# Kernel optimization log

Hardware: AMD Instinct MI355X
Metric: run time of the kernel (lower is better)

## Reference

```python
import jax, jax.numpy as jnp
import numpy as np

B, T, C, H = 8, 2048, 512, 512


def setup_inputs() -> dict:
    key = jax.random.key(0)
    ks = jax.random.split(key, 9)
    s = 1.0 / np.sqrt(C)
    return {
        "q": jax.random.normal(ks[0], (B, T, C), jnp.float32),
        "k": jax.random.normal(ks[1], (B, T, C), jnp.float32),
        "v": jax.random.normal(ks[2], (B, T, C), jnp.float32),
        "Wq": jax.random.normal(ks[3], (C, H), jnp.float32) * s,
        "bq": jax.random.normal(ks[4], (H,), jnp.float32) * 0.01,
        "Wk": jax.random.normal(ks[5], (C, H), jnp.float32) * s,
        "bk": jax.random.normal(ks[6], (H,), jnp.float32) * 0.01,
        "Wv": jax.random.normal(ks[7], (C, H), jnp.float32) * s,
        "bv": jax.random.normal(ks[8], (H,), jnp.float32) * 0.01,
    }


def reference(q, k, v, Wq, bq, Wk, bk, Wv, bv):
    # Linear projections (Real_Linear == nn.Linear): [B,T,C] @ [C,H] + [H]
    query = jnp.einsum('btc,ch->bth', q, Wq) + bq
    key_p = jnp.einsum('btc,ch->bth', k, Wk) + bk
    value = jnp.einsum('btc,ch->bth', v, Wv) + bv
    # energy = Q @ K^T / sqrt(H)  -> [B, T, T]
    energy = jnp.einsum('bth,byh->bty', query, key_p) / jnp.sqrt(jnp.asarray(H, query.dtype))
    attn = jax.nn.softmax(energy, axis=-1)
    # weighted value: [B, T, T] @ [B, T, H] -> [B, T, H]
    return jnp.einsum('bty,byh->bth', attn, value)
```

## Files before the change

### kernel.cpp

```cpp
#include <hip/hip_runtime.h>
#include <hip/hip_bf16.h>

typedef unsigned short u16;
typedef unsigned int u32;
typedef short s16x8 __attribute__((ext_vector_type(8)));
typedef float f32x4 __attribute__((ext_vector_type(4)));

#define NB 8
#define NT 2048
#define NC 512
#define NH 512

__device__ __forceinline__ u16 f2bf(float f) {
  unsigned u = __float_as_uint(f);
  u += 0x7FFFu + ((u >> 16) & 1u);
  return (u16)(u >> 16);
}

__device__ __forceinline__ void gld16(const u16* src, u16* lds_dst) {
  __builtin_amdgcn_global_load_lds(
      (const __attribute__((address_space(1))) u32*)src,
      (__attribute__((address_space(3))) u32*)lds_dst, 16, 0, 0);
}

__global__ __launch_bounds__(256) void wt_kernel(const float* __restrict__ Wq,
                                                 const float* __restrict__ Wk,
                                                 const float* __restrict__ Wv,
                                                 u16* __restrict__ WqT,
                                                 u16* __restrict__ WkT,
                                                 u16* __restrict__ WvT) {
  __shared__ float tile[32][33];
  const float* W = (blockIdx.z == 0) ? Wq : (blockIdx.z == 1) ? Wk : Wv;
  u16* WT = (blockIdx.z == 0) ? WqT : (blockIdx.z == 1) ? WkT : WvT;
  const int x = threadIdx.x & 31;
  const int y = threadIdx.x >> 5;
  const int k0 = blockIdx.x * 32, h0 = blockIdx.y * 32;
#pragma unroll
  for (int p = 0; p < 4; ++p)
    tile[y + 8 * p][x] = W[(size_t)(k0 + y + 8 * p) * NH + h0 + x];
  __syncthreads();
#pragma unroll
  for (int p = 0; p < 4; ++p)
    WT[(size_t)(h0 + y + 8 * p) * NC + k0 + x] = f2bf(tile[x][y + 8 * p]);
}

__global__ __launch_bounds__(256) void proj_kernel(const float* __restrict__ Xq,
                                                   const float* __restrict__ Xk,
                                                   const float* __restrict__ Xv,
                                                   const u16* __restrict__ WqT,
                                                   const u16* __restrict__ WkT,
                                                   const u16* __restrict__ WvT,
                                                   const float* __restrict__ bq,
                                                   const float* __restrict__ bk,
                                                   const float* __restrict__ bv,
                                                   u16* __restrict__ Yq,
                                                   u16* __restrict__ Yk,
                                                   u16* __restrict__ Yv) {
  __shared__ __align__(16) u16 Asub[2][128 * 40];
  __shared__ __align__(16) u16 Bsub[2][128 * 40];
  const int zz = blockIdx.z;
  const float* X = (zz == 0) ? Xq : (zz == 1) ? Xk : Xv;
  const u16* WT = (zz == 0) ? WqT : (zz == 1) ? WkT : WvT;
  const float* bias = (zz == 0) ? bq : (zz == 1) ? bk : bv;
  u16* Y = (zz == 0) ? Yq : (zz == 1) ? Yk : Yv;

  const int t = threadIdx.x;
  const int lane = t & 63;
  const int w = t >> 6;
  const int l16 = lane & 15;
  const int ko8 = (lane >> 4) * 8;
  const int m0 = blockIdx.y * 128;
  const int n0 = blockIdx.x * 128;
  const int wr = (w >> 1) * 64, wc = (w & 1) * 64;
  f32x4 acc[4][4] = {};

  float4 areg[4];
  int4 breg[2];
#define PLOAD(kt)                                                              \
  {                                                                            \
    const int k0_ = (kt) * 32;                                                 \
    _Pragma("unroll")                                                          \
    for (int p = 0; p < 4; ++p) {                                              \
      int c = t + 256 * p;                                                     \
      areg[p] = *(const float4*)&X[(size_t)(m0 + (c >> 3)) * NC + k0_ + (c & 7) * 4]; \
    }                                                                          \
    _Pragma("unroll")                                                          \
    for (int p = 0; p < 2; ++p) {                                              \
      int c = t + 256 * p;                                                     \
      breg[p] = *(const int4*)&WT[(size_t)(n0 + (c >> 2)) * NC + k0_ + (c & 3) * 8];  \
    }                                                                          \
  }
#define PWRITE(buf)                                                            \
  {                                                                            \
    _Pragma("unroll")                                                          \
    for (int p = 0; p < 4; ++p) {                                              \
      int c = t + 256 * p;                                                     \
      ushort4 bb;                                                              \
      bb.x = f2bf(areg[p].x); bb.y = f2bf(areg[p].y);                          \
      bb.z = f2bf(areg[p].z); bb.w = f2bf(areg[p].w);                          \
      *(ushort4*)&Asub[buf][(c >> 3) * 40 + (c & 7) * 4] = bb;                 \
    }                                                                          \
    _Pragma("unroll")                                                          \
    for (int p = 0; p < 2; ++p) {                                              \
      int c = t + 256 * p;                                                     \
      *(int4*)&Bsub[buf][(c >> 2) * 40 + (c & 3) * 8] = breg[p];               \
    }                                                                          \
  }

  PLOAD(0)
  PWRITE(0)
  __syncthreads();

  int pb = 0;
  for (int kt = 0; kt < 16; ++kt) {
    if (kt < 15) PLOAD(kt + 1)
    s16x8 af[4], bf[4];
#pragma unroll
    for (int i = 0; i < 4; ++i)
      af[i] = *(const s16x8*)&Asub[pb][(wr + i * 16 + l16) * 40 + ko8];
#pragma unroll
    for (int j = 0; j < 4; ++j)
      bf[j] = *(const s16x8*)&Bsub[pb][(wc + j * 16 + l16) * 40 + ko8];
#pragma unroll
    for (int i = 0; i < 4; ++i)
#pragma unroll
      for (int j = 0; j < 4; ++j)
        acc[i][j] = __builtin_amdgcn_mfma_f32_16x16x32_bf16(af[i], bf[j], acc[i][j], 0, 0, 0);
    if (kt < 15) PWRITE(pb ^ 1)
    __syncthreads();
    pb ^= 1;
  }
#undef PLOAD
#undef PWRITE
  const int rg = (lane >> 4) * 4;
#pragma unroll
  for (int i = 0; i < 4; ++i)
#pragma unroll
    for (int j = 0; j < 4; ++j) {
      const int col = n0 + wc + j * 16 + l16;
      const float bcol = bias[col];
#pragma unroll
      for (int jj = 0; jj < 4; ++jj) {
        const int row = m0 + wr + i * 16 + rg + jj;
        Y[(size_t)row * NH + col] = f2bf(acc[i][j][jj] + bcol);
      }
    }
}

__global__ __launch_bounds__(256) void vt_kernel(const u16* __restrict__ Vp,
                                                 u16* __restrict__ VpT) {
  __shared__ u16 tile[32][33];
  const int x = threadIdx.x & 31;
  const int y = threadIdx.x >> 5;
  const int t0 = blockIdx.x * 32, h0 = blockIdx.y * 32, b = blockIdx.z;
  const u16* src = Vp + (size_t)b * NT * NH;
  u16* dst = VpT + (size_t)b * NH * NT;
#pragma unroll
  for (int p = 0; p < 4; ++p)
    tile[y + 8 * p][x] = src[(size_t)(t0 + y + 8 * p) * NH + h0 + x];
  __syncthreads();
#pragma unroll
  for (int p = 0; p < 4; ++p)
    dst[(size_t)(h0 + y + 8 * p) * NT + t0 + x] = tile[x][y + 8 * p];
}

__global__ __launch_bounds__(512, 2) void flash_partial(const u16* __restrict__ Qp,
                                                        const u16* __restrict__ Kp,
                                                        const u16* __restrict__ VpT,
                                                        float* __restrict__ O0,
                                                        float* __restrict__ O1,
                                                        float* __restrict__ mlws) {
  __shared__ __align__(16) u16 Klds[2][32 * 512];
  __shared__ __align__(16) u16 Vlds[2][32 * 512];

  const int t = threadIdx.x;
  const int lane = t & 63;
  const int w = t >> 6;
  const int l16 = lane & 15;
  const int g = lane >> 4;
  const int g8 = g * 8;
  const int b = blockIdx.x;
  const int q0 = blockIdx.y * 128;
  const int z = blockIdx.z;
  const int qg = q0 + w * 16 + l16;
  const int kperm = (l16 >> 2) * 8 + (l16 & 3);
  const float kscale = 0.044194173824159216f;

  s16x8 qf[16];
  {
    const u16* qrow = Qp + (size_t)(b * NT + qg) * NH;
#pragma unroll
    for (int ks = 0; ks < 16; ++ks)
      qf[ks] = *(const s16x8*)&qrow[ks * 32 + g8];
  }

  f32x4 oacc[32] = {};
  float m_run = -1e30f, l_run = 0.f;

  const u16* kbat = Kp + (size_t)(b * NT + z * 1024) * NH;
  const u16* vbat = VpT + (size_t)b * NH * NT + z * 1024;

#define STAGE(buf, it)                                                         \
  {                                                                            \
    _Pragma("unroll")                                                          \
    for (int r = 0; r < 4; ++r) {                                              \
      const int i = w * 4 + r;                                      \
      gld16(kbat + (size_t)((it) * 32 + kperm + ((i & 1) << 2)) * NH           \
                 + ((i >> 1) << 5) + g8,                                       \
            &Klds[buf][i * 512]);                                              \
      gld16(vbat + (size_t)(i * 16 + l16) * NT + (it) * 32 + g8,               \
            &Vlds[buf][i * 512]);                                              \
    }                                                                          \
  }

  STAGE(0, 0)
  __syncthreads();

  int pb = 0;
  for (int it = 0; it < 32; ++it) {
    if (it < 31) STAGE(pb ^ 1, it + 1)
    f32x4 s0a = {}, s0b = {}, s1a = {}, s1b = {};
    __builtin_amdgcn_s_setprio(1);
#pragma unroll
    for (int ks = 0; ks < 8; ++ks) {
      s16x8 kf0 = *(const s16x8*)&Klds[pb][(ks * 2 + 0) * 512 + lane * 8];
      s16x8 kf1 = *(const s16x8*)&Klds[pb][(ks * 2 + 1) * 512 + lane * 8];
      s16x8 kf2 = *(const s16x8*)&Klds[pb][((ks + 8) * 2 + 0) * 512 + lane * 8];
      s16x8 kf3 = *(const s16x8*)&Klds[pb][((ks + 8) * 2 + 1) * 512 + lane * 8];
      s0a = __builtin_amdgcn_mfma_f32_16x16x32_bf16(kf0, qf[ks], s0a, 0, 0, 0);
      s1a = __builtin_amdgcn_mfma_f32_16x16x32_bf16(kf1, qf[ks], s1a, 0, 0, 0);
      s0b = __builtin_amdgcn_mfma_f32_16x16x32_bf16(kf2, qf[ks + 8], s0b, 0, 0, 0);
      s1b = __builtin_amdgcn_mfma_f32_16x16x32_bf16(kf3, qf[ks + 8], s1b, 0, 0, 0);
    }
    __builtin_amdgcn_s_setprio(0);
    const f32x4 s0 = s0a + s0b;
    const f32x4 s1 = s1a + s1b;
    float pv[8];
#pragma unroll
    for (int j = 0; j < 4; ++j) { pv[j] = s0[j] * kscale; pv[4 + j] = s1[j] * kscale; }
    float mx = pv[0];
#pragma unroll
    for (int j = 1; j < 8; ++j) mx = fmaxf(mx, pv[j]);
    mx = fmaxf(mx, __shfl_xor(mx, 16, 64));
    mx = fmaxf(mx, __shfl_xor(mx, 32, 64));
    if (__any(mx > m_run + 8.f)) {
      const float m_new = fmaxf(m_run, mx);
      const float scale = __expf(m_run - m_new);
#pragma unroll
      for (int ht = 0; ht < 32; ++ht) {
        oacc[ht][0] *= scale; oacc[ht][1] *= scale;
        oacc[ht][2] *= scale; oacc[ht][3] *= scale;
      }
      l_run *= scale;
      m_run = m_new;
    }
    float ts = 0.f;
#pragma unroll
    for (int j = 0; j < 8; ++j) { pv[j] = __expf(pv[j] - m_run); ts += pv[j]; }
    l_run += ts;
    union { u32 u[4]; s16x8 v; } pf;
    pf.u[0] = ((u32)f2bf(pv[1]) << 16) | f2bf(pv[0]);
    pf.u[1] = ((u32)f2bf(pv[3]) << 16) | f2bf(pv[2]);
    pf.u[2] = ((u32)f2bf(pv[5]) << 16) | f2bf(pv[4]);
    pf.u[3] = ((u32)f2bf(pv[7]) << 16) | f2bf(pv[6]);
    __builtin_amdgcn_s_setprio(1);
#pragma unroll
    for (int ht = 0; ht < 32; ++ht) {
      s16x8 vf = *(const s16x8*)&Vlds[pb][ht * 512 + lane * 8];
      oacc[ht] = __builtin_amdgcn_mfma_f32_16x16x32_bf16(vf, pf.v, oacc[ht], 0, 0, 0);
    }
    __builtin_amdgcn_s_setprio(0);
    __syncthreads();
    pb ^= 1;
  }
  float* obase = (z ? O1 : O0) + (size_t)(b * NT + qg) * NH;
#pragma unroll
  for (int ht = 0; ht < 32; ++ht) {
    float4 st;
    st.x = oacc[ht][0]; st.y = oacc[ht][1];
    st.z = oacc[ht][2]; st.w = oacc[ht][3];
    *(float4*)&obase[ht * 16 + g * 4] = st;
  }
  float lt = l_run;
  lt += __shfl_xor(lt, 16, 64);
  lt += __shfl_xor(lt, 32, 64);
  if (g == 0) {
    const size_t row = (size_t)b * NT + qg;
    mlws[row * 4 + z * 2 + 0] = m_run;
    mlws[row * 4 + z * 2 + 1] = lt;
  }
#undef STAGE
}

__global__ __launch_bounds__(256) void merge_kernel(float* __restrict__ out,
                                                    const float* __restrict__ O1,
                                                    const float* __restrict__ mlws) {
  const size_t row = (size_t)blockIdx.x * 2 + (threadIdx.x >> 7);
  const int col4 = (threadIdx.x & 127) * 4;
  const float m0 = mlws[row * 4 + 0], l0 = mlws[row * 4 + 1];
  const float m1 = mlws[row * 4 + 2], l1 = mlws[row * 4 + 3];
  const float m = fmaxf(m0, m1);
  const float a0 = __expf(m0 - m), a1 = __expf(m1 - m);
  const float inv = 1.f / (a0 * l0 + a1 * l1);
  const float c0 = a0 * inv, c1 = a1 * inv;
  const size_t idx = row * NH + col4;
  float4 o0 = *(const float4*)&out[idx];
  float4 o1 = *(const float4*)&O1[idx];
  float4 r;
  r.x = c0 * o0.x + c1 * o1.x;
  r.y = c0 * o0.y + c1 * o1.y;
  r.z = c0 * o0.z + c1 * o1.z;
  r.w = c0 * o0.w + c1 * o1.w;
  *(float4*)&out[idx] = r;
}

__global__ __launch_bounds__(256, 1) void flash_kernel(const u16* __restrict__ Qp,
                                                       const u16* __restrict__ Kp,
                                                       const u16* __restrict__ VpT,
                                                       float* __restrict__ out) {
  __shared__ __align__(16) u16 Klds[2][32 * 512];
  __shared__ __align__(16) u16 Vlds[2][32 * 512];

  const int t = threadIdx.x;
  const int lane = t & 63;
  const int w = t >> 6;
  const int l16 = lane & 15;
  const int g = lane >> 4;
  const int g8 = g * 8;
  const int b = blockIdx.x;
  const int q0 = blockIdx.y * 64;
  const int qg = q0 + w * 16 + l16;
  const int kperm = (l16 >> 2) * 8 + (l16 & 3);
  const float kscale = 0.044194173824159216f;

  s16x8 qf[16];
  {
    const u16* qrow = Qp + (size_t)(b * NT + qg) * NH;
#pragma unroll
    for (int ks = 0; ks < 16; ++ks)
      qf[ks] = *(const s16x8*)&qrow[ks * 32 + g8];
  }
  f32x4 oacc[32] = {};
  float m_run = -1e30f, l_run = 0.f;
  const u16* kbat = Kp + (size_t)b * NT * NH;
  const u16* vbat = VpT + (size_t)b * NH * NT;

#pragma unroll
  for (int r = 0; r < 8; ++r) {
    const int i = w * 8 + r;
    gld16(kbat + (size_t)(kperm + ((i & 1) << 2)) * NH + ((i >> 1) << 5) + g8,
          &Klds[0][i * 512]);
    gld16(vbat + (size_t)(i * 16 + l16) * NT + g8, &Vlds[0][i * 512]);
  }
  __syncthreads();

  int pb = 0;
  for (int it = 0; it < 64; ++it) {
    if (it < 63) {
      const int kv1 = (it + 1) * 32;
      const int nb = pb ^ 1;
#pragma unroll
      for (int r = 0; r < 8; ++r) {
        const int i = w * 8 + r;
        gld16(kbat + (size_t)(kv1 + kperm + ((i & 1) << 2)) * NH + ((i >> 1) << 5) + g8,
              &Klds[nb][i * 512]);
        gld16(vbat + (size_t)(i * 16 + l16) * NT + kv1 + g8, &Vlds[nb][i * 512]);
      }
    }
    f32x4 s0 = {}, s1 = {};
#pragma unroll
    for (int ks = 0; ks < 16; ++ks) {
      s16x8 kf0 = *(const s16x8*)&Klds[pb][(ks * 2 + 0) * 512 + lane * 8];
      s16x8 kf1 = *(const s16x8*)&Klds[pb][(ks * 2 + 1) * 512 + lane * 8];
      s0 = __builtin_amdgcn_mfma_f32_16x16x32_bf16(kf0, qf[ks], s0, 0, 0, 0);
      s1 = __builtin_amdgcn_mfma_f32_16x16x32_bf16(kf1, qf[ks], s1, 0, 0, 0);
    }
    float pv[8];
#pragma unroll
    for (int j = 0; j < 4; ++j) { pv[j] = s0[j] * kscale; pv[4 + j] = s1[j] * kscale; }
    float mx = pv[0];
#pragma unroll
    for (int j = 1; j < 8; ++j) mx = fmaxf(mx, pv[j]);
    mx = fmaxf(mx, __shfl_xor(mx, 16, 64));
    mx = fmaxf(mx, __shfl_xor(mx, 32, 64));
    if (__any(mx > m_run + 8.f)) {
      const float m_new = fmaxf(m_run, mx);
      const float scale = __expf(m_run - m_new);
#pragma unroll
      for (int ht = 0; ht < 32; ++ht) {
        oacc[ht][0] *= scale; oacc[ht][1] *= scale;
        oacc[ht][2] *= scale; oacc[ht][3] *= scale;
      }
      l_run *= scale;
      m_run = m_new;
    }
    float ts = 0.f;
#pragma unroll
    for (int j = 0; j < 8; ++j) { pv[j] = __expf(pv[j] - m_run); ts += pv[j]; }
    l_run += ts;
    union { u32 u[4]; s16x8 v; } pf;
    pf.u[0] = ((u32)f2bf(pv[1]) << 16) | f2bf(pv[0]);
    pf.u[1] = ((u32)f2bf(pv[3]) << 16) | f2bf(pv[2]);
    pf.u[2] = ((u32)f2bf(pv[5]) << 16) | f2bf(pv[4]);
    pf.u[3] = ((u32)f2bf(pv[7]) << 16) | f2bf(pv[6]);
#pragma unroll
    for (int ht = 0; ht < 32; ++ht) {
      s16x8 vf = *(const s16x8*)&Vlds[pb][ht * 512 + lane * 8];
      oacc[ht] = __builtin_amdgcn_mfma_f32_16x16x32_bf16(vf, pf.v, oacc[ht], 0, 0, 0);
    }
    __syncthreads();
    pb ^= 1;
  }
  float lt = l_run;
  lt += __shfl_xor(lt, 16, 64);
  lt += __shfl_xor(lt, 32, 64);
  const float inv = 1.f / lt;
  float* obase = out + (size_t)(b * NT + qg) * NH;
#pragma unroll
  for (int ht = 0; ht < 32; ++ht) {
    float4 st;
    st.x = oacc[ht][0] * inv; st.y = oacc[ht][1] * inv;
    st.z = oacc[ht][2] * inv; st.w = oacc[ht][3] * inv;
    *(float4*)&obase[ht * 16 + g * 4] = st;
  }
}

extern "C" void kernel_launch(void* const* d_in, const int* in_sizes, int n_in,
                              void* d_out, int out_size, void* d_ws, size_t ws_size,
                              hipStream_t stream) {
  (void)in_sizes; (void)n_in; (void)out_size;
  const float* q  = (const float*)d_in[0];
  const float* k  = (const float*)d_in[1];
  const float* v  = (const float*)d_in[2];
  const float* Wq = (const float*)d_in[3];
  const float* bq = (const float*)d_in[4];
  const float* Wk = (const float*)d_in[5];
  const float* bk = (const float*)d_in[6];
  const float* Wv = (const float*)d_in[7];
  const float* bv = (const float*)d_in[8];
  float* out = (float*)d_out;

  u16* ws   = (u16*)d_ws;
  u16* WqT  = ws;
  u16* WkT  = WqT + (size_t)NC * NH;
  u16* WvT  = WkT + (size_t)NC * NH;
  u16* Qp   = WvT + (size_t)NC * NH;
  u16* Kp   = Qp + (size_t)NB * NT * NH;
  u16* Vp   = Kp + (size_t)NB * NT * NH;
  u16* VpT  = Vp + (size_t)NB * NT * NH;
  u16* endb = VpT + (size_t)NB * NT * NH;
  float* O1   = (float*)endb;
  float* mlws = O1 + (size_t)NB * NT * NH;
  const size_t need = (size_t)((char*)(mlws + (size_t)NB * NT * 4) - (char*)d_ws);

  wt_kernel<<<dim3(16, 16, 3), 256, 0, stream>>>(Wq, Wk, Wv, WqT, WkT, WvT);

  proj_kernel<<<dim3(4, 128, 3), 256, 0, stream>>>(q, k, v, WqT, WkT, WvT,
                                                   bq, bk, bv, Qp, Kp, Vp);

  vt_kernel<<<dim3(64, 16, NB), 256, 0, stream>>>(Vp, VpT);

  if (ws_size >= need) {
    flash_partial<<<dim3(NB, NT / 128, 2), 512, 0, stream>>>(Qp, Kp, VpT, out, O1, mlws);
    merge_kernel<<<dim3(NB * NT / 2), 256, 0, stream>>>(out, O1, mlws);
  } else {
    flash_kernel<<<dim3(NB, NT / 64), 256, 0, stream>>>(Qp, Kp, VpT, out);
  }
}
```

Before: 215.2 us.

## Switch flash attention to 32x32x16 MFMA with wave-pair split of head dimension

```diff
diff --git a/kernel.cpp b/kernel.cpp
--- a/kernel.cpp
+++ b/kernel.cpp
@@ -5,6 +5,7 @@
 typedef unsigned int u32;
 typedef short s16x8 __attribute__((ext_vector_type(8)));
 typedef float f32x4 __attribute__((ext_vector_type(4)));
+typedef float f32x16 __attribute__((ext_vector_type(16)));
 
 #define NB 8
 #define NT 2048
@@ -172,29 +173,32 @@
                                                         float* __restrict__ mlws) {
   __shared__ __align__(16) u16 Klds[2][32 * 512];
   __shared__ __align__(16) u16 Vlds[2][32 * 512];
+  __shared__ __align__(16) float Sx[8][1024];
 
   const int t = threadIdx.x;
   const int lane = t & 63;
   const int w = t >> 6;
-  const int l16 = lane & 15;
-  const int g = lane >> 4;
-  const int g8 = g * 8;
+  const int qgrp = w >> 1;
+  const int wh = w & 1;
+  const int l31 = lane & 31;
+  const int hi = lane >> 5;
   const int b = blockIdx.x;
   const int q0 = blockIdx.y * 128;
   const int z = blockIdx.z;
-  const int qg = q0 + w * 16 + l16;
-  const int kperm = (l16 >> 2) * 8 + (l16 & 3);
+  const int qg = q0 + qgrp * 32 + l31;
   const float kscale = 0.044194173824159216f;
+  const int kvr = ((l31 >> 4) & 1) * 16 + ((l31 >> 2) & 1) * 8 +
+                  ((l31 >> 3) & 1) * 4 + (l31 & 3);
 
   s16x8 qf[16];
   {
-    const u16* qrow = Qp + (size_t)(b * NT + qg) * NH;
-#pragma unroll
-    for (int ks = 0; ks < 16; ++ks)
-      qf[ks] = *(const s16x8*)&qrow[ks * 32 + g8];
-  }
-
-  f32x4 oacc[32] = {};
+    const u16* qrow = Qp + (size_t)(b * NT + qg) * NH + wh * 256 + hi * 8;
+#pragma unroll
+    for (int f = 0; f < 16; ++f)
+      qf[f] = *(const s16x8*)&qrow[f * 16];
+  }
+
+  f32x16 oacc[8] = {};
   float m_run = -1e30f, l_run = 0.f;
 
   const u16* kbat = Kp + (size_t)(b * NT + z * 1024) * NH;
@@ -203,13 +207,14 @@
 #define STAGE(buf, it)                                                         \
   {                                                                            \
     _Pragma("unroll")                                                          \
-    for (int r = 0; r < 4; ++r) {                                              \
-      const int i = w * 4 + r;                                      \
-      gld16(kbat + (size_t)((it) * 32 + kperm + ((i & 1) << 2)) * NH           \
-                 + ((i >> 1) << 5) + g8,                                       \
-            &Klds[buf][i * 512]);                                              \
-      gld16(vbat + (size_t)(i * 16 + l16) * NT + (it) * 32 + g8,               \
-            &Vlds[buf][i * 512]);                                              \
+    for (int r_ = 0; r_ < 4; ++r_) {                                           \
+      const int f = w * 4 + r_;                                     \
+      gld16(kbat + (size_t)((it) * 32 + kvr) * NH + f * 16 + hi * 8,           \
+            &Klds[buf][f * 512]);                                              \
+      const int whv = f >> 4, htv = (f >> 1) & 7, sv = f & 1;                  \
+      gld16(vbat + (size_t)(whv * 256 + htv * 32 + l31) * NT                   \
+                 + (it) * 32 + sv * 16 + hi * 8,                               \
+            &Vlds[buf][f * 512]);                                              \
     }                                                                          \
   }
 
@@ -219,72 +224,84 @@
   int pb = 0;
   for (int it = 0; it < 32; ++it) {
     if (it < 31) STAGE(pb ^ 1, it + 1)
-    f32x4 s0a = {}, s0b = {}, s1a = {}, s1b = {};
+    f32x16 sacc = {};
     __builtin_amdgcn_s_setprio(1);
 #pragma unroll
-    for (int ks = 0; ks < 8; ++ks) {
-      s16x8 kf0 = *(const s16x8*)&Klds[pb][(ks * 2 + 0) * 512 + lane * 8];
-      s16x8 kf1 = *(const s16x8*)&Klds[pb][(ks * 2 + 1) * 512 + lane * 8];
-      s16x8 kf2 = *(const s16x8*)&Klds[pb][((ks + 8) * 2 + 0) * 512 + lane * 8];
-      s16x8 kf3 = *(const s16x8*)&Klds[pb][((ks + 8) * 2 + 1) * 512 + lane * 8];
-      s0a = __builtin_amdgcn_mfma_f32_16x16x32_bf16(kf0, qf[ks], s0a, 0, 0, 0);
-      s1a = __builtin_amdgcn_mfma_f32_16x16x32_bf16(kf1, qf[ks], s1a, 0, 0, 0);
-      s0b = __builtin_amdgcn_mfma_f32_16x16x32_bf16(kf2, qf[ks + 8], s0b, 0, 0, 0);
-      s1b = __builtin_amdgcn_mfma_f32_16x16x32_bf16(kf3, qf[ks + 8], s1b, 0, 0, 0);
+    for (int f = 0; f < 16; ++f) {
+      s16x8 kf = *(const s16x8*)&Klds[pb][(wh * 16 + f) * 512 + lane * 8];
+      sacc = __builtin_amdgcn_mfma_f32_32x32x16_bf16(kf, qf[f], sacc, 0, 0, 0);
     }
     __builtin_amdgcn_s_setprio(0);
-    const f32x4 s0 = s0a + s0b;
-    const f32x4 s1 = s1a + s1b;
-    float pv[8];
-#pragma unroll
-    for (int j = 0; j < 4; ++j) { pv[j] = s0[j] * kscale; pv[4 + j] = s1[j] * kscale; }
+    {
+      float* myx = &Sx[w][0];
+#pragma unroll
+      for (int c = 0; c < 4; ++c) {
+        float4 tv;
+        tv.x = sacc[c * 4 + 0]; tv.y = sacc[c * 4 + 1];
+        tv.z = sacc[c * 4 + 2]; tv.w = sacc[c * 4 + 3];
+        *(float4*)&myx[c * 256 + lane * 4] = tv;
+      }
+    }
+    __syncthreads();
+    float pv[16];
+    {
+      const float* twx = &Sx[w ^ 1][0];
+#pragma unroll
+      for (int c = 0; c < 4; ++c) {
+        float4 tv = *(const float4*)&twx[c * 256 + lane * 4];
+        pv[c * 4 + 0] = (sacc[c * 4 + 0] + tv.x) * kscale;
+        pv[c * 4 + 1] = (sacc[c * 4 + 1] + tv.y) * kscale;
+        pv[c * 4 + 2] = (sacc[c * 4 + 2] + tv.z) * kscale;
+        pv[c * 4 + 3] = (sacc[c * 4 + 3] + tv.w) * kscale;
+      }
+    }
     float mx = pv[0];
 #pragma unroll
-    for (int j = 1; j < 8; ++j) mx = fmaxf(mx, pv[j]);
-    mx = fmaxf(mx, __shfl_xor(mx, 16, 64));
+    for (int j = 1; j < 16; ++j) mx = fmaxf(mx, pv[j]);
     mx = fmaxf(mx, __shfl_xor(mx, 32, 64));
     if (__any(mx > m_run + 8.f)) {
       const float m_new = fmaxf(m_run, mx);
       const float scale = __expf(m_run - m_new);
 #pragma unroll
-      for (int ht = 0; ht < 32; ++ht) {
-        oacc[ht][0] *= scale; oacc[ht][1] *= scale;
-        oacc[ht][2] *= scale; oacc[ht][3] *= scale;
-      }
+      for (int o = 0; o < 8; ++o) oacc[o] *= scale;
       l_run *= scale;
       m_run = m_new;
     }
     float ts = 0.f;
 #pragma unroll
-    for (int j = 0; j < 8; ++j) { pv[j] = __expf(pv[j] - m_run); ts += pv[j]; }
+    for (int j = 0; j < 16; ++j) { pv[j] = __expf(pv[j] - m_run); ts += pv[j]; }
     l_run += ts;
-    union { u32 u[4]; s16x8 v; } pf;
-    pf.u[0] = ((u32)f2bf(pv[1]) << 16) | f2bf(pv[0]);
-    pf.u[1] = ((u32)f2bf(pv[3]) << 16) | f2bf(pv[2]);
-    pf.u[2] = ((u32)f2bf(pv[5]) << 16) | f2bf(pv[4]);
-    pf.u[3] = ((u32)f2bf(pv[7]) << 16) | f2bf(pv[6]);
+    union { u32 u[4]; s16x8 v; } pf1, pf2;
+#pragma unroll
+    for (int c = 0; c < 4; ++c) {
+      pf1.u[c] = ((u32)f2bf(pv[c * 2 + 1]) << 16) | f2bf(pv[c * 2]);
+      pf2.u[c] = ((u32)f2bf(pv[8 + c * 2 + 1]) << 16) | f2bf(pv[8 + c * 2]);
+    }
     __builtin_amdgcn_s_setprio(1);
 #pragma unroll
-    for (int ht = 0; ht < 32; ++ht) {
-      s16x8 vf = *(const s16x8*)&Vlds[pb][ht * 512 + lane * 8];
-      oacc[ht] = __builtin_amdgcn_mfma_f32_16x16x32_bf16(vf, pf.v, oacc[ht], 0, 0, 0);
+    for (int ht = 0; ht < 8; ++ht) {
+      s16x8 vf1 = *(const s16x8*)&Vlds[pb][(wh * 16 + ht * 2 + 0) * 512 + lane * 8];
+      s16x8 vf2 = *(const s16x8*)&Vlds[pb][(wh * 16 + ht * 2 + 1) * 512 + lane * 8];
+      oacc[ht] = __builtin_amdgcn_mfma_f32_32x32x16_bf16(vf1, pf1.v, oacc[ht], 0, 0, 0);
+      oacc[ht] = __builtin_amdgcn_mfma_f32_32x32x16_bf16(vf2, pf2.v, oacc[ht], 0, 0, 0);
     }
     __builtin_amdgcn_s_setprio(0);
     __syncthreads();
     pb ^= 1;
   }
-  float* obase = (z ? O1 : O0) + (size_t)(b * NT + qg) * NH;
-#pragma unroll
-  for (int ht = 0; ht < 32; ++ht) {
-    float4 st;
-    st.x = oacc[ht][0]; st.y = oacc[ht][1];
-    st.z = oacc[ht][2]; st.w = oacc[ht][3];
-    *(float4*)&obase[ht * 16 + g * 4] = st;
-  }
-  float lt = l_run;
-  lt += __shfl_xor(lt, 16, 64);
-  lt += __shfl_xor(lt, 32, 64);
-  if (g == 0) {
+  float* obase = (z ? O1 : O0) + (size_t)(b * NT + qg) * NH + wh * 256;
+#pragma unroll
+  for (int ht = 0; ht < 8; ++ht) {
+#pragma unroll
+    for (int c = 0; c < 4; ++c) {
+      float4 st;
+      st.x = oacc[ht][c * 4 + 0]; st.y = oacc[ht][c * 4 + 1];
+      st.z = oacc[ht][c * 4 + 2]; st.w = oacc[ht][c * 4 + 3];
+      *(float4*)&obase[ht * 32 + c * 8 + hi * 4] = st;
+    }
+  }
+  float lt = l_run + __shfl_xor(l_run, 32, 64);
+  if (wh == 0 && hi == 0) {
     const size_t row = (size_t)b * NT + qg;
     mlws[row * 4 + z * 2 + 0] = m_run;
     mlws[row * 4 + z * 2 + 1] = lt;
```

Result: slower. 231.8 us (+7.7%).

## Shrink flash_partial to 64-query blocks with 16-key tiles and 16x16x16 PV MFMA

Applied to the files above, without the earlier changes.

```diff
diff --git a/kernel.cpp b/kernel.cpp
--- a/kernel.cpp
+++ b/kernel.cpp
@@ -4,12 +4,19 @@
 typedef unsigned short u16;
 typedef unsigned int u32;
 typedef short s16x8 __attribute__((ext_vector_type(8)));
+typedef short s16x4 __attribute__((ext_vector_type(4)));
 typedef float f32x4 __attribute__((ext_vector_type(4)));
 
 #define NB 8
 #define NT 2048
 #define NC 512
 #define NH 512
+
+#if __has_builtin(__builtin_amdgcn_mfma_f32_16x16x16_bf16)
+#define MFMA_PV(va, pb, c) __builtin_amdgcn_mfma_f32_16x16x16_bf16(va, pb, c, 0, 0, 0)
+#else
+#define MFMA_PV(va, pb, c) __builtin_amdgcn_mfma_f32_16x16x16bf16_1k(va, pb, c, 0, 0, 0)
+#endif
 
 __device__ __forceinline__ u16 f2bf(float f) {
   unsigned u = __float_as_uint(f);
@@ -164,14 +171,14 @@
     dst[(size_t)(h0 + y + 8 * p) * NT + t0 + x] = tile[x][y + 8 * p];
 }
 
-__global__ __launch_bounds__(512, 2) void flash_partial(const u16* __restrict__ Qp,
+__global__ __launch_bounds__(256, 2) void flash_partial(const u16* __restrict__ Qp,
                                                         const u16* __restrict__ Kp,
                                                         const u16* __restrict__ VpT,
                                                         float* __restrict__ O0,
                                                         float* __restrict__ O1,
                                                         float* __restrict__ mlws) {
-  __shared__ __align__(16) u16 Klds[2][32 * 512];
-  __shared__ __align__(16) u16 Vlds[2][32 * 512];
+  __shared__ __align__(16) u16 Klds[2][16 * 512];
+  __shared__ __align__(16) u16 Vlds[2][512 * 16];
 
   const int t = threadIdx.x;
   const int lane = t & 63;
@@ -180,10 +187,9 @@
   const int g = lane >> 4;
   const int g8 = g * 8;
   const int b = blockIdx.x;
-  const int q0 = blockIdx.y * 128;
+  const int q0 = blockIdx.y * 64;
   const int z = blockIdx.z;
   const int qg = q0 + w * 16 + l16;
-  const int kperm = (l16 >> 2) * 8 + (l16 & 3);
   const float kscale = 0.044194173824159216f;
 
   s16x8 qf[16];
@@ -200,47 +206,41 @@
   const u16* kbat = Kp + (size_t)(b * NT + z * 1024) * NH;
   const u16* vbat = VpT + (size_t)b * NH * NT + z * 1024;
 
-#define STAGE(buf, it)                                                         \
-  {                                                                            \
-    _Pragma("unroll")                                                          \
-    for (int r = 0; r < 4; ++r) {                                              \
-      const int i = w * 4 + r;                                      \
-      gld16(kbat + (size_t)((it) * 32 + kperm + ((i & 1) << 2)) * NH           \
-                 + ((i >> 1) << 5) + g8,                                       \
-            &Klds[buf][i * 512]);                                              \
-      gld16(vbat + (size_t)(i * 16 + l16) * NT + (it) * 32 + g8,               \
-            &Vlds[buf][i * 512]);                                              \
-    }                                                                          \
+#define STAGE(buf, it)                                                          \
+  {                                                                             \
+    _Pragma("unroll")                                                           \
+    for (int r = 0; r < 4; ++r) {                                               \
+      const int i = w * 4 + r;                                       \
+                                     \
+      gld16(kbat + (size_t)((it) * 16 + l16) * NH + i * 32 + g8,                \
+            &Klds[buf][i * 512]);                                               \
+                                      \
+      gld16(vbat + (size_t)(i * 32 + (lane >> 1)) * NT + (it) * 16 + (lane & 1) * 8, \
+            &Vlds[buf][i * 512]);                                               \
+    }                                                                           \
   }
 
   STAGE(0, 0)
   __syncthreads();
 
   int pb = 0;
-  for (int it = 0; it < 32; ++it) {
-    if (it < 31) STAGE(pb ^ 1, it + 1)
-    f32x4 s0a = {}, s0b = {}, s1a = {}, s1b = {};
+  for (int it = 0; it < 64; ++it) {
+    if (it < 63) STAGE(pb ^ 1, it + 1)
+    f32x4 sa = {}, sb = {};
     __builtin_amdgcn_s_setprio(1);
 #pragma unroll
     for (int ks = 0; ks < 8; ++ks) {
-      s16x8 kf0 = *(const s16x8*)&Klds[pb][(ks * 2 + 0) * 512 + lane * 8];
-      s16x8 kf1 = *(const s16x8*)&Klds[pb][(ks * 2 + 1) * 512 + lane * 8];
-      s16x8 kf2 = *(const s16x8*)&Klds[pb][((ks + 8) * 2 + 0) * 512 + lane * 8];
-      s16x8 kf3 = *(const s16x8*)&Klds[pb][((ks + 8) * 2 + 1) * 512 + lane * 8];
-      s0a = __builtin_amdgcn_mfma_f32_16x16x32_bf16(kf0, qf[ks], s0a, 0, 0, 0);
-      s1a = __builtin_amdgcn_mfma_f32_16x16x32_bf16(kf1, qf[ks], s1a, 0, 0, 0);
-      s0b = __builtin_amdgcn_mfma_f32_16x16x32_bf16(kf2, qf[ks + 8], s0b, 0, 0, 0);
-      s1b = __builtin_amdgcn_mfma_f32_16x16x32_bf16(kf3, qf[ks + 8], s1b, 0, 0, 0);
+      s16x8 kf0 = *(const s16x8*)&Klds[pb][ks * 512 + lane * 8];
+      s16x8 kf1 = *(const s16x8*)&Klds[pb][(ks + 8) * 512 + lane * 8];
+      sa = __builtin_amdgcn_mfma_f32_16x16x32_bf16(kf0, qf[ks], sa, 0, 0, 0);
+      sb = __builtin_amdgcn_mfma_f32_16x16x32_bf16(kf1, qf[ks + 8], sb, 0, 0, 0);
     }
     __builtin_amdgcn_s_setprio(0);
-    const f32x4 s0 = s0a + s0b;
-    const f32x4 s1 = s1a + s1b;
-    float pv[8];
-#pragma unroll
-    for (int j = 0; j < 4; ++j) { pv[j] = s0[j] * kscale; pv[4 + j] = s1[j] * kscale; }
-    float mx = pv[0];
-#pragma unroll
-    for (int j = 1; j < 8; ++j) mx = fmaxf(mx, pv[j]);
+    const f32x4 s0 = sa + sb;
+    float pv[4];
+#pragma unroll
+    for (int j = 0; j < 4; ++j) pv[j] = s0[j] * kscale;
+    float mx = fmaxf(fmaxf(pv[0], pv[1]), fmaxf(pv[2], pv[3]));
     mx = fmaxf(mx, __shfl_xor(mx, 16, 64));
     mx = fmaxf(mx, __shfl_xor(mx, 32, 64));
     if (__any(mx > m_run + 8.f)) {
@@ -256,18 +256,16 @@
     }
     float ts = 0.f;
 #pragma unroll
-    for (int j = 0; j < 8; ++j) { pv[j] = __expf(pv[j] - m_run); ts += pv[j]; }
+    for (int j = 0; j < 4; ++j) { pv[j] = __expf(pv[j] - m_run); ts += pv[j]; }
     l_run += ts;
-    union { u32 u[4]; s16x8 v; } pf;
+    union { u32 u[2]; s16x4 v; } pf;
     pf.u[0] = ((u32)f2bf(pv[1]) << 16) | f2bf(pv[0]);
     pf.u[1] = ((u32)f2bf(pv[3]) << 16) | f2bf(pv[2]);
-    pf.u[2] = ((u32)f2bf(pv[5]) << 16) | f2bf(pv[4]);
-    pf.u[3] = ((u32)f2bf(pv[7]) << 16) | f2bf(pv[6]);
     __builtin_amdgcn_s_setprio(1);
 #pragma unroll
     for (int ht = 0; ht < 32; ++ht) {
-      s16x8 vf = *(const s16x8*)&Vlds[pb][ht * 512 + lane * 8];
-      oacc[ht] = __builtin_amdgcn_mfma_f32_16x16x32_bf16(vf, pf.v, oacc[ht], 0, 0, 0);
+      s16x4 vf = *(const s16x4*)&Vlds[pb][ht * 256 + l16 * 16 + g * 4];
+      oacc[ht] = MFMA_PV(vf, pf.v, oacc[ht]);
     }
     __builtin_amdgcn_s_setprio(0);
     __syncthreads();
@@ -461,7 +459,7 @@
   vt_kernel<<<dim3(64, 16, NB), 256, 0, stream>>>(Vp, VpT);
 
   if (ws_size >= need) {
-    flash_partial<<<dim3(NB, NT / 128, 2), 512, 0, stream>>>(Qp, Kp, VpT, out, O1, mlws);
+    flash_partial<<<dim3(NB, NT / 64, 2), 256, 0, stream>>>(Qp, Kp, VpT, out, O1, mlws);
     merge_kernel<<<dim3(NB * NT / 2), 256, 0, stream>>>(out, O1, mlws);
   } else {
     flash_kernel<<<dim3(NB, NT / 64), 256, 0, stream>>>(Qp, Kp, VpT, out);
```

After: 275.8 us. 28.2% more time.
